# Kernel tuning notes

Measured on AMD Instinct MI355X. Metric: run time of the kernel, lower is better.

## Reference

```python
import jax, jax.numpy as jnp
import numpy as np

DT = 0.05
TAU = 0.15
SIGMA = float(np.sqrt(2.0 * DT / TAU))  # GaussianNoise default sigma
NOISE_SCALE = 1.0

N = 2048        # nneurons
RANK = 64       # nbg
BATCH = 2048
IN_DIM = 128    # input_sources['stim'] size


def setup_inputs() -> dict:
    key = jax.random.key(0)
    ks = jax.random.split(key, 10)
    inv_sqrt_n = 1.0 / np.sqrt(N)
    return {
        "r_thalamic": jax.random.uniform(ks[0], (BATCH, RANK), jnp.float32),
        "stim": jax.random.normal(ks[1], (BATCH, IN_DIM), jnp.float32),
        "x": jax.random.normal(ks[2], (BATCH, N), jnp.float32) * inv_sqrt_n,
        "r": jax.nn.softplus(jax.random.normal(ks[3], (BATCH, N), jnp.float32) * inv_sqrt_n),
        "J": jax.random.normal(ks[4], (N, N), jnp.float32) * (1.2 * inv_sqrt_n),
        "B": jax.random.normal(ks[5], (1, N), jnp.float32),
        "U": jax.random.normal(ks[6], (N, RANK), jnp.float32) * inv_sqrt_n,
        "V": jax.random.normal(ks[7], (RANK, N), jnp.float32) * inv_sqrt_n,
        "I_stim": jax.random.normal(ks[8], (IN_DIM, N), jnp.float32) * inv_sqrt_n,
        "eps": jax.random.normal(ks[9], (BATCH, N), jnp.float32),
    }


def reference(r_thalamic, stim, x, r, J, B, U, V, I_stim, eps):
    # external input: stim @ I['stim']  -> (batch, N)
    ext = stim @ I_stim
    # bg_tensor @ r == U @ diag(r_thalamic) @ V @ r, computed in low-rank form:
    # (batch, rank) * (batch, rank) -> project back with U
    rec_input = (r_thalamic * (r @ V.T)) @ U.T          # (batch, N)
    pre = -x + r @ J + rec_input + B + ext               # (batch, N)
    noisy = pre + (SIGMA * NOISE_SCALE) * eps            # GaussianNoise
    x_new = x + (DT / TAU) * noisy
    r_new = jax.nn.softplus(x_new)
    return (x_new, r_new)
```

## Files before the change

### kernel.cpp

```cpp
#include <hip/hip_runtime.h>
#include <cstdint>
#include <cstddef>


#define KA 2176
#define KB 2240
#define NN 2048

using frag_ab = __attribute__((ext_vector_type(8))) short;
using frag_cd = __attribute__((ext_vector_type(4))) float;

__device__ __forceinline__ unsigned short f2bf(float f) {
  union { float f; unsigned int i; } v;
  v.f = f;
  unsigned int r = v.i + 0x7fffu + ((v.i >> 16) & 1u);
  return (unsigned short)(r >> 16);
}

__device__ __forceinline__ uint4 cvt8(const float* __restrict__ p) {
  float4 a = *(const float4*)p;
  float4 b = *(const float4*)(p + 4);
  union { uint4 v; unsigned short u[8]; } d;
  d.u[0] = f2bf(a.x); d.u[1] = f2bf(a.y); d.u[2] = f2bf(a.z); d.u[3] = f2bf(a.w);
  d.u[4] = f2bf(b.x); d.u[5] = f2bf(b.y); d.u[6] = f2bf(b.z); d.u[7] = f2bf(b.w);
  return d.v;
}

__device__ __forceinline__ void gl_lds16(const void* g, void* l) {
  __builtin_amdgcn_global_load_lds(
      (const __attribute__((address_space(1))) void*)g,
      (__attribute__((address_space(3))) void*)l, 16, 0, 0);
}

__global__ __launch_bounds__(256) void prep(
    const float* __restrict__ J, const float* __restrict__ Ist,
    const float* __restrict__ rg, const float* __restrict__ stim,
    const float* __restrict__ U, const float* __restrict__ V,
    unsigned short* __restrict__ Ap, unsigned short* __restrict__ Bp,
    float* __restrict__ part) {
  __shared__ unsigned short tile[64 * 66];
  __shared__ alignas(16) unsigned short Ats[32 * 64];
  __shared__ alignas(16) unsigned short Bts[64 * 64];
  const int blk = blockIdx.x;
  const int t = threadIdx.x;

  if (blk < 1088) {
    const float* src;
    int dst_off, cx, cy;
    if (blk < 1024) { src = J;   dst_off = 0;    cx = blk & 31; cy = blk >> 5; }
    else            { src = Ist; dst_off = 2048; cx = (blk - 1024) & 31; cy = (blk - 1024) >> 5; }
    const int r0 = cy * 64, c0 = cx * 64;
    const int sr = t >> 3, c8 = t & 7;
#pragma unroll
    for (int p = 0; p < 2; ++p) {
      const int row = sr + 32 * p;
      union { uint4 v; unsigned short u[8]; } d;
      d.v = cvt8(&src[(size_t)(r0 + row) * 2048 + c0 + c8 * 8]);
#pragma unroll
      for (int e = 0; e < 8; ++e) tile[row * 66 + c8 * 8 + e] = d.u[e];
    }
    __syncthreads();
#pragma unroll
    for (int p = 0; p < 2; ++p) {
      const int scol = sr + 32 * p;
      union { uint4 v; unsigned short u[8]; } d;
#pragma unroll
      for (int e = 0; e < 8; ++e) d.u[e] = tile[(c8 * 8 + e) * 66 + scol];
      *(uint4*)&Bp[(size_t)(c0 + scol) * KB + dst_off + r0 + c8 * 8] = d.v;
    }
  } else if (blk < 1216) {
    const int row = (blk - 1088) * 16 + (t >> 4);
    const int ch  = t & 15;
    *(uint4*)&Ap[(size_t)row * KA + 2048 + ch * 8] =
        cvt8(&stim[(size_t)row * 128 + ch * 8]);
  } else if (blk < 1280) {
    const int row = (blk - 1216) * 32 + (t >> 3);
    const int ch  = t & 7;
    *(uint4*)&Bp[(size_t)row * KB + 2176 + ch * 8] =
        cvt8(&U[(size_t)row * 64 + ch * 8]);
  } else {
    const int tb = blk - 1280;
    const int mt = tb & 63, s = tb >> 6;
    const int b0 = mt * 32;
    const int wave = t >> 6, lane = t & 63;
    const int q = lane >> 4, l15 = lane & 15;
    const int arow = t >> 3, ac8 = t & 7;

    const float* gA  = rg + (size_t)(b0 + arow) * 2048 + s * 512 + ac8 * 8;
    const float* gB0 = V  + (size_t)arow        * 2048 + s * 512 + ac8 * 8;
    const float* gB1 = V  + (size_t)(arow + 32) * 2048 + s * 512 + ac8 * 8;
    unsigned short* pAp = Ap + (size_t)(b0 + arow) * KA + s * 512 + ac8 * 8;

    frag_cd acc0 = {0.f, 0.f, 0.f, 0.f};
    frag_cd acc1 = {0.f, 0.f, 0.f, 0.f};

    for (int kt = 0; kt < 8; ++kt) {
      const int k0 = kt * 64;
      uint4 va  = cvt8(gA + k0);
      uint4 vb0 = cvt8(gB0 + k0);
      uint4 vb1 = cvt8(gB1 + k0);
      *(uint4*)&pAp[k0] = va;
      __syncthreads();
      *(uint4*)&Ats[t * 8]        = va;
      *(uint4*)&Bts[t * 8]        = vb0;
      *(uint4*)&Bts[2048 + t * 8] = vb1;
      __syncthreads();
#pragma unroll
      for (int ks = 0; ks < 2; ++ks) {
        frag_ab a0 = *(const frag_ab*)&Ats[(l15)      * 64 + ks * 32 + q * 8];
        frag_ab a1 = *(const frag_ab*)&Ats[(16 + l15) * 64 + ks * 32 + q * 8];
        frag_ab b  = *(const frag_ab*)&Bts[(wave * 16 + l15) * 64 + ks * 32 + q * 8];
        acc0 = __builtin_amdgcn_mfma_f32_16x16x32_bf16(a0, b, acc0, 0, 0, 0);
        acc1 = __builtin_amdgcn_mfma_f32_16x16x32_bf16(a1, b, acc1, 0, 0, 0);
      }
    }
    const int p = wave * 16 + l15;
#pragma unroll
    for (int reg = 0; reg < 4; ++reg) {
      const int m0 = q * 4 + reg;
      part[((size_t)s * 2048 + b0 + m0) * 64 + p]      = acc0[reg];
      part[((size_t)s * 2048 + b0 + m0 + 16) * 64 + p] = acc1[reg];
    }
  }
}

__global__ __launch_bounds__(256, 4) void main_gemm(
    const unsigned short* __restrict__ Ap, const unsigned short* __restrict__ Bp,
    const float* __restrict__ part, const float* __restrict__ tha,
    const float* __restrict__ xg, const float* __restrict__ epsg,
    const float* __restrict__ Bvec,
    float* __restrict__ outx, float* __restrict__ outr) {
  __shared__ alignas(16) unsigned short As[2][64 * 64];
  __shared__ alignas(16) unsigned short Bs[2][64 * 64];

  const int t = threadIdx.x;
  const int wave = t >> 6, lane = t & 63;
  const int q = lane >> 4, l15 = lane & 15, l7 = lane & 7;
  const int wm = (wave & 1) * 32, wn = (wave >> 1) * 32;

  const int bid = blockIdx.x;
  const int xcd = bid & 7, idx = bid >> 3;
  const int mt = ((xcd >> 2) << 4) + (idx >> 3);
  const int nt = ((xcd & 3) << 3) + (idx & 7);
  const int bm0 = mt * 64, bn0 = nt * 64;

  const unsigned short* gA[2];
  const unsigned short* gB[2];
  uint4 tval[2];
#pragma unroll
  for (int r = 0; r < 2; ++r) {
    const int ci = r * 256 + t;
    const int row = ci >> 3;
    const int lc = (ci & 7) ^ (row & 7);
    gA[r] = Ap + (size_t)(bm0 + row) * KA + lc * 8;
    gB[r] = Bp + (size_t)(bn0 + row) * KB + lc * 8;

    const int p0 = lc * 8;
    const size_t base = ((size_t)(bm0 + row)) * 64 + p0;
    float4 s0 = *(const float4*)&part[base];
    float4 s1 = *(const float4*)&part[base + 4];
#pragma unroll
    for (int s = 1; s < 4; ++s) {
      float4 a = *(const float4*)&part[(size_t)s * 131072 + base];
      float4 b = *(const float4*)&part[(size_t)s * 131072 + base + 4];
      s0.x += a.x; s0.y += a.y; s0.z += a.z; s0.w += a.w;
      s1.x += b.x; s1.y += b.y; s1.z += b.z; s1.w += b.w;
    }
    float4 th0 = *(const float4*)&tha[base];
    float4 th1 = *(const float4*)&tha[base + 4];
    union { uint4 v; unsigned short u[8]; } d;
    d.u[0] = f2bf(th0.x * s0.x); d.u[1] = f2bf(th0.y * s0.y);
    d.u[2] = f2bf(th0.z * s0.z); d.u[3] = f2bf(th0.w * s0.w);
    d.u[4] = f2bf(th1.x * s1.x); d.u[5] = f2bf(th1.y * s1.y);
    d.u[6] = f2bf(th1.z * s1.z); d.u[7] = f2bf(th1.w * s1.w);
    tval[r] = d.v;
  }

  frag_cd acc[2][2];
#pragma unroll
  for (int i = 0; i < 2; ++i)
#pragma unroll
    for (int j = 0; j < 2; ++j) {
      frag_cd z = {0.f, 0.f, 0.f, 0.f};
      acc[i][j] = z;
    }

  asm volatile("s_waitcnt vmcnt(0)" ::: "memory");
#pragma unroll
  for (int r = 0; r < 2; ++r) {
    gl_lds16(gA[r], &As[0][(size_t)(r * 256 + wave * 64) * 8]);
    gl_lds16(gB[r], &Bs[0][(size_t)(r * 256 + wave * 64) * 8]);
  }

#pragma unroll 1
  for (int kt = 0; kt < 34; ++kt) {
    const int cur = kt & 1;
    asm volatile("s_waitcnt lgkmcnt(0)" ::: "memory");
    __builtin_amdgcn_s_barrier();
    __builtin_amdgcn_sched_barrier(0);
    if (kt < 33) {
      const int k0n = (kt + 1) * 64;
      unsigned short* dA = &As[cur ^ 1][0];
      unsigned short* dB = &Bs[cur ^ 1][0];
#pragma unroll
      for (int r = 0; r < 2; ++r) {
        gl_lds16(gA[r] + k0n, dA + (size_t)(r * 256 + wave * 64) * 8);
        gl_lds16(gB[r] + k0n, dB + (size_t)(r * 256 + wave * 64) * 8);
      }
      asm volatile("s_waitcnt vmcnt(4)" ::: "memory");
    } else {
      unsigned short* dA = &As[cur ^ 1][0];
      unsigned short* dB = &Bs[cur ^ 1][0];
#pragma unroll
      for (int r = 0; r < 2; ++r) {
        *(uint4*)&dA[(size_t)(r * 256 + t) * 8] = tval[r];
        gl_lds16(gB[r] + 34 * 64, dB + (size_t)(r * 256 + wave * 64) * 8);
      }
      asm volatile("s_waitcnt vmcnt(2) lgkmcnt(0)" ::: "memory");
    }
    __builtin_amdgcn_s_barrier();
    __builtin_amdgcn_sched_barrier(0);
    const unsigned short* cA = &As[cur][0];
    const unsigned short* cB = &Bs[cur][0];
#pragma unroll
    for (int ks = 0; ks < 2; ++ks) {
      const int lc = ks * 4 + q;
      frag_ab af[2], bfr[2];
#pragma unroll
      for (int i = 0; i < 2; ++i) {
        af[i]  = *(const frag_ab*)&cA[(wm + i * 16 + l15) * 64 + ((lc ^ l7) * 8)];
        bfr[i] = *(const frag_ab*)&cB[(wn + i * 16 + l15) * 64 + ((lc ^ l7) * 8)];
      }
#pragma unroll
      for (int i = 0; i < 2; ++i)
#pragma unroll
        for (int j = 0; j < 2; ++j)
          acc[i][j] = __builtin_amdgcn_mfma_f32_16x16x32_bf16(af[i], bfr[j], acc[i][j], 0, 0, 0);
    }
  }

  {
    asm volatile("s_waitcnt vmcnt(0) lgkmcnt(0)" ::: "memory");
    __builtin_amdgcn_s_barrier();
    __builtin_amdgcn_sched_barrier(0);
    const unsigned short* cA = &As[0][0];
    const unsigned short* cB = &Bs[0][0];
#pragma unroll
    for (int ks = 0; ks < 2; ++ks) {
      const int lc = ks * 4 + q;
      frag_ab af[2], bfr[2];
#pragma unroll
      for (int i = 0; i < 2; ++i) {
        af[i]  = *(const frag_ab*)&cA[(wm + i * 16 + l15) * 64 + ((lc ^ l7) * 8)];
        bfr[i] = *(const frag_ab*)&cB[(wn + i * 16 + l15) * 64 + ((lc ^ l7) * 8)];
      }
#pragma unroll
      for (int i = 0; i < 2; ++i)
#pragma unroll
        for (int j = 0; j < 2; ++j)
          acc[i][j] = __builtin_amdgcn_mfma_f32_16x16x32_bf16(af[i], bfr[j], acc[i][j], 0, 0, 0);
    }
  }

  const float A_DT = 0.33333334f;
  const float SIG  = 0.81649658092772615f;
#pragma unroll
  for (int j = 0; j < 2; ++j) {
    const int nc = bn0 + wn + j * 16 + l15;
    const float bvf = Bvec[nc];
#pragma unroll
    for (int i = 0; i < 2; ++i) {
#pragma unroll
      for (int reg = 0; reg < 4; ++reg) {
        const int mr = bm0 + wm + i * 16 + q * 4 + reg;
        const size_t off = (size_t)mr * NN + nc;
        const float xf = xg[off];
        const float ef = epsg[off];
        const float xn = xf + A_DT * (acc[i][j][reg] + bvf - xf + SIG * ef);
        outx[off] = xn;
        outr[off] = (xn > 20.f) ? xn : log1pf(__expf(xn));
      }
    }
  }
}

extern "C" void kernel_launch(void* const* d_in, const int* in_sizes, int n_in,
                              void* d_out, int out_size, void* d_ws, size_t ws_size,
                              hipStream_t stream) {
  (void)in_sizes; (void)n_in; (void)out_size; (void)ws_size;
  const float* tha  = (const float*)d_in[0];
  const float* stim = (const float*)d_in[1];
  const float* x    = (const float*)d_in[2];
  const float* r    = (const float*)d_in[3];
  const float* J    = (const float*)d_in[4];
  const float* Bv   = (const float*)d_in[5];
  const float* U    = (const float*)d_in[6];
  const float* V    = (const float*)d_in[7];
  const float* Ist  = (const float*)d_in[8];
  const float* eps  = (const float*)d_in[9];

  unsigned short* Apk = (unsigned short*)d_ws;
  unsigned short* Bpk = Apk + (size_t)NN * KA;
  float* part = (float*)(Bpk + (size_t)NN * KB);
  float* outx = (float*)d_out;
  float* outr = outx + (size_t)NN * NN;

  prep<<<1536, 256, 0, stream>>>(J, Ist, r, stim, U, V, Apk, Bpk, part);
  main_gemm<<<1024, 256, 0, stream>>>(Apk, Bpk, part, tha, x, eps, Bv,
                                      outx, outr);
}
```

Before: 176.8 us.

## Replace double-buffered BK=64 loop with single-buffered BK=128 tiles

```diff
diff --git a/kernel.cpp b/kernel.cpp
--- a/kernel.cpp
+++ b/kernel.cpp
@@ -130,8 +130,8 @@
     const float* __restrict__ xg, const float* __restrict__ epsg,
     const float* __restrict__ Bvec,
     float* __restrict__ outx, float* __restrict__ outr) {
-  __shared__ alignas(16) unsigned short As[2][64 * 64];
-  __shared__ alignas(16) unsigned short Bs[2][64 * 64];
+  __shared__ alignas(16) unsigned short As[64 * 128];
+  __shared__ alignas(16) unsigned short Bs[64 * 128];
 
   const int t = threadIdx.x;
   const int wave = t >> 6, lane = t & 63;
@@ -144,16 +144,25 @@
   const int nt = ((xcd & 3) << 3) + (idx & 7);
   const int bm0 = mt * 64, bn0 = nt * 64;
 
-  const unsigned short* gA[2];
-  const unsigned short* gB[2];
+  const unsigned short* gA[4];
+  const unsigned short* gB[4];
+#pragma unroll
+  for (int r = 0; r < 4; ++r) {
+    const int ci = r * 256 + t;
+    const int row = ci >> 4;
+    const int lc = (ci & 15) ^ (row & 15);
+    gA[r] = Ap + (size_t)(bm0 + row) * KA + lc * 8;
+    gB[r] = Bp + (size_t)(bn0 + row) * KB + lc * 8;
+  }
+
   uint4 tval[2];
+  const unsigned short* gU[2];
 #pragma unroll
   for (int r = 0; r < 2; ++r) {
     const int ci = r * 256 + t;
     const int row = ci >> 3;
     const int lc = (ci & 7) ^ (row & 7);
-    gA[r] = Ap + (size_t)(bm0 + row) * KA + lc * 8;
-    gB[r] = Bp + (size_t)(bn0 + row) * KB + lc * 8;
+    gU[r] = Bp + (size_t)(bn0 + row) * KB + 2176 + lc * 8;
 
     const int p0 = lc * 8;
     const size_t base = ((size_t)(bm0 + row)) * 64 + p0;
@@ -185,51 +194,23 @@
       acc[i][j] = z;
     }
 
-  asm volatile("s_waitcnt vmcnt(0)" ::: "memory");
-#pragma unroll
-  for (int r = 0; r < 2; ++r) {
-    gl_lds16(gA[r], &As[0][(size_t)(r * 256 + wave * 64) * 8]);
-    gl_lds16(gB[r], &Bs[0][(size_t)(r * 256 + wave * 64) * 8]);
-  }
-
 #pragma unroll 1
-  for (int kt = 0; kt < 34; ++kt) {
-    const int cur = kt & 1;
-    asm volatile("s_waitcnt lgkmcnt(0)" ::: "memory");
-    __builtin_amdgcn_s_barrier();
-    __builtin_amdgcn_sched_barrier(0);
-    if (kt < 33) {
-      const int k0n = (kt + 1) * 64;
-      unsigned short* dA = &As[cur ^ 1][0];
-      unsigned short* dB = &Bs[cur ^ 1][0];
-#pragma unroll
-      for (int r = 0; r < 2; ++r) {
-        gl_lds16(gA[r] + k0n, dA + (size_t)(r * 256 + wave * 64) * 8);
-        gl_lds16(gB[r] + k0n, dB + (size_t)(r * 256 + wave * 64) * 8);
-      }
-      asm volatile("s_waitcnt vmcnt(4)" ::: "memory");
-    } else {
-      unsigned short* dA = &As[cur ^ 1][0];
-      unsigned short* dB = &Bs[cur ^ 1][0];
-#pragma unroll
-      for (int r = 0; r < 2; ++r) {
-        *(uint4*)&dA[(size_t)(r * 256 + t) * 8] = tval[r];
-        gl_lds16(gB[r] + 34 * 64, dB + (size_t)(r * 256 + wave * 64) * 8);
-      }
-      asm volatile("s_waitcnt vmcnt(2) lgkmcnt(0)" ::: "memory");
-    }
-    __builtin_amdgcn_s_barrier();
-    __builtin_amdgcn_sched_barrier(0);
-    const unsigned short* cA = &As[cur][0];
-    const unsigned short* cB = &Bs[cur][0];
-#pragma unroll
-    for (int ks = 0; ks < 2; ++ks) {
-      const int lc = ks * 4 + q;
+  for (int kt = 0; kt < 17; ++kt) {
+    const int k0 = kt * 128;
+    __syncthreads();
+#pragma unroll
+    for (int r = 0; r < 4; ++r) {
+      gl_lds16(gA[r] + k0, &As[(size_t)(r * 256 + wave * 64) * 8]);
+      gl_lds16(gB[r] + k0, &Bs[(size_t)(r * 256 + wave * 64) * 8]);
+    }
+    __syncthreads();
+#pragma unroll
+    for (int ks = 0; ks < 4; ++ks) {
       frag_ab af[2], bfr[2];
 #pragma unroll
       for (int i = 0; i < 2; ++i) {
-        af[i]  = *(const frag_ab*)&cA[(wm + i * 16 + l15) * 64 + ((lc ^ l7) * 8)];
-        bfr[i] = *(const frag_ab*)&cB[(wn + i * 16 + l15) * 64 + ((lc ^ l7) * 8)];
+        af[i]  = *(const frag_ab*)&As[(wm + i * 16 + l15) * 128 + (((ks * 4 + q) ^ l15) * 8)];
+        bfr[i] = *(const frag_ab*)&Bs[(wn + i * 16 + l15) * 128 + (((ks * 4 + q) ^ l15) * 8)];
       }
 #pragma unroll
       for (int i = 0; i < 2; ++i)
@@ -240,19 +221,20 @@
   }
 
   {
-    asm volatile("s_waitcnt vmcnt(0) lgkmcnt(0)" ::: "memory");
-    __builtin_amdgcn_s_barrier();
-    __builtin_amdgcn_sched_barrier(0);
-    const unsigned short* cA = &As[0][0];
-    const unsigned short* cB = &Bs[0][0];
+    __syncthreads();
+#pragma unroll
+    for (int r = 0; r < 2; ++r) {
+      *(uint4*)&As[(size_t)(r * 256 + t) * 8] = tval[r];
+      gl_lds16(gU[r], &Bs[(size_t)(r * 256 + wave * 64) * 8]);
+    }
+    __syncthreads();
 #pragma unroll
     for (int ks = 0; ks < 2; ++ks) {
-      const int lc = ks * 4 + q;
       frag_ab af[2], bfr[2];
 #pragma unroll
       for (int i = 0; i < 2; ++i) {
-        af[i]  = *(const frag_ab*)&cA[(wm + i * 16 + l15) * 64 + ((lc ^ l7) * 8)];
-        bfr[i] = *(const frag_ab*)&cB[(wn + i * 16 + l15) * 64 + ((lc ^ l7) * 8)];
+        af[i]  = *(const frag_ab*)&As[(wm + i * 16 + l15) * 64 + (((ks * 4 + q) ^ l7) * 8)];
+        bfr[i] = *(const frag_ab*)&Bs[(wn + i * 16 + l15) * 64 + (((ks * 4 + q) ^ l7) * 8)];
       }
 #pragma unroll
       for (int i = 0; i < 2; ++i)
```

Measured after the change: 197.1 us. 11.5% more time.

## Split main GEMM K-loop across two sequential launches with partial-sum buffer

Applied to the files above, without the earlier changes.

```diff
diff --git a/kernel.cpp b/kernel.cpp
--- a/kernel.cpp
+++ b/kernel.cpp
@@ -129,7 +129,8 @@
     const float* __restrict__ part, const float* __restrict__ tha,
     const float* __restrict__ xg, const float* __restrict__ epsg,
     const float* __restrict__ Bvec,
-    float* __restrict__ outx, float* __restrict__ outr) {
+    float* outx, float* __restrict__ outr,
+    const float* p0, float* pout, const int kt0, const int mode) {
   __shared__ alignas(16) unsigned short As[2][64 * 64];
   __shared__ alignas(16) unsigned short Bs[2][64 * 64];
 
@@ -146,7 +147,7 @@
 
   const unsigned short* gA[2];
   const unsigned short* gB[2];
-  uint4 tval[2];
+  uint4 tval[2] = {{0u, 0u, 0u, 0u}, {0u, 0u, 0u, 0u}};
 #pragma unroll
   for (int r = 0; r < 2; ++r) {
     const int ci = r * 256 + t;
@@ -155,25 +156,27 @@
     gA[r] = Ap + (size_t)(bm0 + row) * KA + lc * 8;
     gB[r] = Bp + (size_t)(bn0 + row) * KB + lc * 8;
 
-    const int p0 = lc * 8;
-    const size_t base = ((size_t)(bm0 + row)) * 64 + p0;
-    float4 s0 = *(const float4*)&part[base];
-    float4 s1 = *(const float4*)&part[base + 4];
-#pragma unroll
-    for (int s = 1; s < 4; ++s) {
-      float4 a = *(const float4*)&part[(size_t)s * 131072 + base];
-      float4 b = *(const float4*)&part[(size_t)s * 131072 + base + 4];
-      s0.x += a.x; s0.y += a.y; s0.z += a.z; s0.w += a.w;
-      s1.x += b.x; s1.y += b.y; s1.z += b.z; s1.w += b.w;
-    }
-    float4 th0 = *(const float4*)&tha[base];
-    float4 th1 = *(const float4*)&tha[base + 4];
-    union { uint4 v; unsigned short u[8]; } d;
-    d.u[0] = f2bf(th0.x * s0.x); d.u[1] = f2bf(th0.y * s0.y);
-    d.u[2] = f2bf(th0.z * s0.z); d.u[3] = f2bf(th0.w * s0.w);
-    d.u[4] = f2bf(th1.x * s1.x); d.u[5] = f2bf(th1.y * s1.y);
-    d.u[6] = f2bf(th1.z * s1.z); d.u[7] = f2bf(th1.w * s1.w);
-    tval[r] = d.v;
+    if (mode) {
+      const int p0c = lc * 8;
+      const size_t base = ((size_t)(bm0 + row)) * 64 + p0c;
+      float4 s0 = *(const float4*)&part[base];
+      float4 s1 = *(const float4*)&part[base + 4];
+#pragma unroll
+      for (int s = 1; s < 4; ++s) {
+        float4 a = *(const float4*)&part[(size_t)s * 131072 + base];
+        float4 b = *(const float4*)&part[(size_t)s * 131072 + base + 4];
+        s0.x += a.x; s0.y += a.y; s0.z += a.z; s0.w += a.w;
+        s1.x += b.x; s1.y += b.y; s1.z += b.z; s1.w += b.w;
+      }
+      float4 th0 = *(const float4*)&tha[base];
+      float4 th1 = *(const float4*)&tha[base + 4];
+      union { uint4 v; unsigned short u[8]; } d;
+      d.u[0] = f2bf(th0.x * s0.x); d.u[1] = f2bf(th0.y * s0.y);
+      d.u[2] = f2bf(th0.z * s0.z); d.u[3] = f2bf(th0.w * s0.w);
+      d.u[4] = f2bf(th1.x * s1.x); d.u[5] = f2bf(th1.y * s1.y);
+      d.u[6] = f2bf(th1.z * s1.z); d.u[7] = f2bf(th1.w * s1.w);
+      tval[r] = d.v;
+    }
   }
 
   frag_cd acc[2][2];
@@ -186,20 +189,23 @@
     }
 
   asm volatile("s_waitcnt vmcnt(0)" ::: "memory");
-#pragma unroll
-  for (int r = 0; r < 2; ++r) {
-    gl_lds16(gA[r], &As[0][(size_t)(r * 256 + wave * 64) * 8]);
-    gl_lds16(gB[r], &Bs[0][(size_t)(r * 256 + wave * 64) * 8]);
+  {
+    const int k0 = kt0 * 64;
+#pragma unroll
+    for (int r = 0; r < 2; ++r) {
+      gl_lds16(gA[r] + k0, &As[0][(size_t)(r * 256 + wave * 64) * 8]);
+      gl_lds16(gB[r] + k0, &Bs[0][(size_t)(r * 256 + wave * 64) * 8]);
+    }
   }
 
 #pragma unroll 1
-  for (int kt = 0; kt < 34; ++kt) {
+  for (int kt = 0; kt < 17; ++kt) {
     const int cur = kt & 1;
     asm volatile("s_waitcnt lgkmcnt(0)" ::: "memory");
     __builtin_amdgcn_s_barrier();
     __builtin_amdgcn_sched_barrier(0);
-    if (kt < 33) {
-      const int k0n = (kt + 1) * 64;
+    if (kt < 16) {
+      const int k0n = (kt0 + kt + 1) * 64;
       unsigned short* dA = &As[cur ^ 1][0];
       unsigned short* dB = &Bs[cur ^ 1][0];
 #pragma unroll
@@ -208,7 +214,7 @@
         gl_lds16(gB[r] + k0n, dB + (size_t)(r * 256 + wave * 64) * 8);
       }
       asm volatile("s_waitcnt vmcnt(4)" ::: "memory");
-    } else {
+    } else if (mode) {
       unsigned short* dA = &As[cur ^ 1][0];
       unsigned short* dB = &Bs[cur ^ 1][0];
 #pragma unroll
@@ -217,6 +223,8 @@
         gl_lds16(gB[r] + 34 * 64, dB + (size_t)(r * 256 + wave * 64) * 8);
       }
       asm volatile("s_waitcnt vmcnt(2) lgkmcnt(0)" ::: "memory");
+    } else {
+      asm volatile("s_waitcnt vmcnt(0)" ::: "memory");
     }
     __builtin_amdgcn_s_barrier();
     __builtin_amdgcn_sched_barrier(0);
@@ -239,12 +247,12 @@
     }
   }
 
-  {
+  if (mode) {
     asm volatile("s_waitcnt vmcnt(0) lgkmcnt(0)" ::: "memory");
     __builtin_amdgcn_s_barrier();
     __builtin_amdgcn_sched_barrier(0);
-    const unsigned short* cA = &As[0][0];
-    const unsigned short* cB = &Bs[0][0];
+    const unsigned short* cA = &As[1][0];
+    const unsigned short* cB = &Bs[1][0];
 #pragma unroll
     for (int ks = 0; ks < 2; ++ks) {
       const int lc = ks * 4 + q;
@@ -260,25 +268,40 @@
         for (int j = 0; j < 2; ++j)
           acc[i][j] = __builtin_amdgcn_mfma_f32_16x16x32_bf16(af[i], bfr[j], acc[i][j], 0, 0, 0);
     }
-  }
-
-  const float A_DT = 0.33333334f;
-  const float SIG  = 0.81649658092772615f;
-#pragma unroll
-  for (int j = 0; j < 2; ++j) {
-    const int nc = bn0 + wn + j * 16 + l15;
-    const float bvf = Bvec[nc];
-#pragma unroll
-    for (int i = 0; i < 2; ++i) {
-#pragma unroll
-      for (int reg = 0; reg < 4; ++reg) {
-        const int mr = bm0 + wm + i * 16 + q * 4 + reg;
-        const size_t off = (size_t)mr * NN + nc;
-        const float xf = xg[off];
-        const float ef = epsg[off];
-        const float xn = xf + A_DT * (acc[i][j][reg] + bvf - xf + SIG * ef);
-        outx[off] = xn;
-        outr[off] = (xn > 20.f) ? xn : log1pf(__expf(xn));
+
+    const float A_DT = 0.33333334f;
+    const float SIG  = 0.81649658092772615f;
+#pragma unroll
+    for (int j = 0; j < 2; ++j) {
+      const int nc = bn0 + wn + j * 16 + l15;
+      const float bvf = Bvec[nc];
+#pragma unroll
+      for (int i = 0; i < 2; ++i) {
+#pragma unroll
+        for (int reg = 0; reg < 4; ++reg) {
+          const int mr = bm0 + wm + i * 16 + q * 4 + reg;
+          const size_t off = (size_t)mr * NN + nc;
+          const float pv = p0[off];
+          const float xf = xg[off];
+          const float ef = epsg[off];
+          const float xn =
+              xf + A_DT * (acc[i][j][reg] + pv + bvf - xf + SIG * ef);
+          outx[off] = xn;
+          outr[off] = (xn > 20.f) ? xn : log1pf(__expf(xn));
+        }
+      }
+    }
+  } else {
+#pragma unroll
+    for (int j = 0; j < 2; ++j) {
+      const int nc = bn0 + wn + j * 16 + l15;
+#pragma unroll
+      for (int i = 0; i < 2; ++i) {
+#pragma unroll
+        for (int reg = 0; reg < 4; ++reg) {
+          const int mr = bm0 + wm + i * 16 + q * 4 + reg;
+          pout[(size_t)mr * NN + nc] = acc[i][j][reg];
+        }
       }
     }
   }
@@ -307,5 +330,7 @@
 
   prep<<<1536, 256, 0, stream>>>(J, Ist, r, stim, U, V, Apk, Bpk, part);
   main_gemm<<<1024, 256, 0, stream>>>(Apk, Bpk, part, tha, x, eps, Bv,
-                                      outx, outr);
-}
+                                      outx, outr, nullptr, outx, 0, 0);
+  main_gemm<<<1024, 256, 0, stream>>>(Apk, Bpk, part, tha, x, eps, Bv,
+                                      outx, outr, outx, nullptr, 17, 1);
+}
```

After: 184.1 us. 4.1% more time.
